# Kernel tuning notes

Measured on AMD Instinct MI355X. Metric: run time of the kernel, lower is better.

The kernel has to match this reference:

```python
import jax, jax.numpy as jnp
import numpy as np

DIM = 512
HEADS = 4
DH = 128          # dim_head
CHUNK = 16        # chunk_size
MAX_LR = 0.01     # default_adaptive_step_transform max_lr
EPS = 1e-6        # flax RMSNorm epsilon


def setup_inputs() -> dict:
    key = jax.random.key(0)
    ks = jax.random.split(key, 8)
    B, S = 2, 2048
    dim_inner = HEADS * DH
    seq = jax.random.normal(ks[0], (B, S, DIM), jnp.float32)
    store_norm_scale = jnp.ones((DIM,), jnp.float32)               # RMSNorm scale
    W_kv = (jax.random.normal(ks[1], (DIM, 2 * dim_inner)) * 0.02).astype(jnp.float32)
    W_step = (jax.random.normal(ks[2], (DIM, HEADS)) * 0.02).astype(jnp.float32)
    W_mom = (jax.random.normal(ks[3], (DIM, HEADS)) * 0.02).astype(jnp.float32)
    W_decay = (jax.random.normal(ks[4], (DIM, HEADS)) * 0.02).astype(jnp.float32)
    # past memory-MLP weights, shared init expanded to (b, h, dh, dh)
    w0 = jnp.broadcast_to((jax.random.normal(ks[5], (DH, DH)) * 0.02).astype(jnp.float32), (B, HEADS, DH, DH)) + 0.0
    w1 = jnp.broadcast_to((jax.random.normal(ks[6], (DH, DH)) * 0.02).astype(jnp.float32), (B, HEADS, DH, DH)) + 0.0
    return {"seq": seq, "store_norm_scale": store_norm_scale, "W_kv": W_kv,
            "W_step": W_step, "W_mom": W_mom, "W_decay": W_decay, "w0": w0, "w1": w1}


def _mlp(w0, w1, x):
    # MemoryMLP depth=2: x @ w0 ; silu ; @ w1
    return jax.nn.silu(x @ w0) @ w1


def _chunk_loss(w0, w1, k, lr, v):
    pred = _mlp(w0, w1, k)                       # [c, d]
    return jnp.sum(jnp.mean((pred - v) ** 2, axis=-1) * lr)


def _binop(e1, e2):
    a1, b1 = e1
    a2, b2 = e2
    return a1 * a2, a2 * b1 + b2


def _lin_scan(a, b):
    # first-order linear recurrence y_t = a_t * y_{t-1} + b_t along chunk axis (axis=2)
    return jax.lax.associative_scan(_binop, (a, b), axis=2)[1]


def _store(seq, store_norm_scale, W_kv, W_step, W_mom, W_decay, w0, w1):
    B, S, _ = seq.shape
    n = S // CHUNK
    # pre RMSNorm (with scale)
    x = seq * jax.lax.rsqrt(jnp.mean(seq * seq, axis=-1, keepdims=True) + EPS) * store_norm_scale
    # adaptive per-token lr:  sigmoid(x @ W_step) * max_lr  -> [b, h, s]
    lr = jax.nn.sigmoid(jnp.einsum('bsd,dh->bhs', x, W_step)) * MAX_LR
    # per-chunk mean -> momentum / decay factors  [b, h, n, 1]
    mean = x.reshape(B, n, CHUNK, DIM).mean(axis=2)
    mom = jax.nn.sigmoid(jnp.einsum('bnd,dh->bhn', mean, W_mom))[..., None]
    dec = jax.nn.sigmoid(jnp.einsum('bnd,dh->bhn', mean, W_decay))[..., None]
    # keys / values  [b*h, n, c, dh]
    kv = x @ W_kv
    k, v = jnp.split(kv, 2, axis=-1)
    k = k.reshape(B, n, CHUNK, HEADS, DH).transpose(0, 3, 1, 2, 4).reshape(B * HEADS, n, CHUNK, DH)
    v = v.reshape(B, n, CHUNK, HEADS, DH).transpose(0, 3, 1, 2, 4).reshape(B * HEADS, n, CHUNK, DH)
    lr_ch = lr.reshape(B, HEADS, n, CHUNK).reshape(B * HEADS, n, CHUNK)
    w0bh = w0.reshape(B * HEADS, DH, DH)
    w1bh = w1.reshape(B * HEADS, DH, DH)
    # per-chunk gradients of the MLP loss at the *past* weights (all chunks independent)
    gfn = jax.grad(_chunk_loss, argnums=(0, 1))
    gfn = jax.vmap(gfn, in_axes=(None, None, 0, 0, 0))   # over chunks n
    gfn = jax.vmap(gfn, in_axes=(0, 0, 0, 0, 0))         # over b*h
    g0, g1 = gfn(w0bh, w1bh, k, lr_ch, v)                # [b*h, n, dh, dh]
    s0 = (-g0).reshape(B, HEADS, n, DH * DH)             # surprises
    s1 = (-g1).reshape(B, HEADS, n, DH * DH)
    # momentum scan then decay scan (Titans update rule)
    m0 = _lin_scan(jnp.broadcast_to(mom, s0.shape), s0)
    m1 = _lin_scan(jnp.broadcast_to(mom, s1.shape), s1)
    u0 = _lin_scan(jnp.broadcast_to(1.0 - dec, m0.shape), m0)
    u1 = _lin_scan(jnp.broadcast_to(1.0 - dec, m1.shape), m1)
    updates = jnp.stack([u0.reshape(B, HEADS, n, DH, DH),
                         u1.reshape(B, HEADS, n, DH, DH)], axis=0)  # [2, b, h, n, dh, dh]
    return updates


def reference(seq, store_norm_scale, W_kv, W_step, W_mom, W_decay, w0, w1):
    return _store(seq, store_norm_scale, W_kv, W_step, W_mom, W_decay, w0, w1)
```

## Files before the change

### kernel.cpp

```cpp
#include <hip/hip_runtime.h>

#define DIMX 512
#define HEADSX 4
#define DHX 128
#define CHX 16
#define NCX 128
#define SX 2048
#define BX 2
#define BHX 8
#define PADX 520
#define PADF 136

typedef unsigned short ushort_t;
typedef unsigned int uint_t;
typedef short bf16x8 __attribute__((ext_vector_type(8)));
typedef float f32x4 __attribute__((ext_vector_type(4)));

__device__ __forceinline__ float sigmoidf_(float z){ return 1.0f/(1.0f + __expf(-z)); }

__device__ __forceinline__ ushort_t f2bf(float f){
  uint_t u = __float_as_uint(f);
  return (ushort_t)((u + 0x7FFFu + ((u >> 16) & 1u)) >> 16);
}
__device__ __forceinline__ uint_t pk2(float a, float b){
  return (uint_t)f2bf(a) | ((uint_t)f2bf(b) << 16);
}

__global__ __launch_bounds__(256) void k_prep(const float* __restrict__ Wkv,
    const float* __restrict__ w0, const float* __restrict__ w1,
    ushort_t* __restrict__ WkvT, ushort_t* __restrict__ w0T,
    ushort_t* __restrict__ w1T, ushort_t* __restrict__ w1n){
  int blk = blockIdx.x; int tid = threadIdx.x;
  if (blk < 64){
    int h = blk >> 4, kt = blk & 15;
    __shared__ ushort_t tile[256][33];
    for (int i=tid; i<8192; i+=256){
      int kk = i >> 8, col = i & 255;
      int wcol = (col < 128) ? (h*128 + col) : (384 + h*128 + col);
      float v = Wkv[(size_t)(kt*32+kk)*1024 + wcol];
      tile[col][kk] = f2bf(v);
    }
    __syncthreads();
    for (int i=tid; i<8192; i+=256){
      int col = i >> 5, kk = i & 31;
      WkvT[(((size_t)h*16 + kt)*256 + col)*32 + kk] = tile[col][kk];
    }
  } else {
    int bh = blk - 64;
    size_t base = (size_t)bh*16384;
    for (int i=tid; i<16384; i+=256){
      int r = i >> 7, c = i & 127;
      w0T[base + i] = f2bf(w0[base + (size_t)c*128 + r]);
      w1T[base + i] = f2bf(w1[base + (size_t)c*128 + r]);
      w1n[base + i] = f2bf(w1[base + i]);
    }
  }
}

__global__ __launch_bounds__(256) void k_fused2(const float* __restrict__ seq,
    const float* __restrict__ scale, const float* __restrict__ Wstep,
    const float* __restrict__ Wmom, const float* __restrict__ Wdec,
    const ushort_t* __restrict__ WkvT, const ushort_t* __restrict__ w0T,
    const ushort_t* __restrict__ w1T, const ushort_t* __restrict__ w1n,
    ushort_t* __restrict__ fac0, ushort_t* __restrict__ fac1,
    float* __restrict__ momw, float* __restrict__ decw){
  int blk = blockIdx.x;
  int bh = blk & 7, t = blk >> 3;
  int b = bh >> 2, h = bh & 3;
  int bt = bh*NCX + t;
  __shared__ __align__(16) ushort_t xs[16*PADX];
  __shared__ __align__(16) ushort_t ks[16*PADF];
  __shared__ __align__(16) ushort_t as_[16*PADF];
  __shared__ __align__(16) ushort_t dp_[16*PADF];
  __shared__ __align__(16) ushort_t dh_[16*PADF];
  __shared__ float red[4][8][4];
  __shared__ float rs_s[16], lr_s[16];
  int tid = threadIdx.x;
  int wv = tid>>6, lane = tid&63;
  int quad = lane>>4, nl = lane&15;
  const f32x4 zero = {0.f,0.f,0.f,0.f};

  const float4* sb = (const float4*)(seq + ((size_t)(b*SX + t*CHX))*DIMX);
  float4 q[8];
  #pragma unroll
  for (int it=0; it<8; it++) q[it] = sb[tid + 256*it];
  int k4 = tid & 127; int d0 = k4*4;
  float4 sc4 = *(const float4*)(scale + d0);
  float wsv[4], wmv[4], wdv[4];
  #pragma unroll
  for (int j=0;j<4;j++){
    wsv[j] = Wstep[(d0+j)*4 + h];
    wmv[j] = Wmom [(d0+j)*4 + h];
    wdv[j] = Wdec [(d0+j)*4 + h];
  }
  #pragma unroll
  for (int it=0; it<8; it++){
    float ssp = q[it].x*q[it].x + q[it].y*q[it].y + q[it].z*q[it].z + q[it].w*q[it].w;
    float xwx = q[it].x*sc4.x, xwy = q[it].y*sc4.y;
    float xwz = q[it].z*sc4.z, xww = q[it].w*sc4.w;
    float lp = xwx*wsv[0] + xwy*wsv[1] + xwz*wsv[2] + xww*wsv[3];
    float pm = xwx*wmv[0] + xwy*wmv[1] + xwz*wmv[2] + xww*wmv[3];
    float pd = xwx*wdv[0] + xwy*wdv[1] + xwz*wdv[2] + xww*wdv[3];
    #pragma unroll
    for (int o=32;o>0;o>>=1){
      ssp += __shfl_down(ssp,o,64); lp += __shfl_down(lp,o,64);
      pm  += __shfl_down(pm,o,64);  pd += __shfl_down(pd,o,64);
    }
    if (lane==0){ red[wv][it][0]=ssp; red[wv][it][1]=lp; red[wv][it][2]=pm; red[wv][it][3]=pd; }
  }
  __syncthreads();
  if (tid < 16){
    int c = tid;
    int w0i = (c & 1) ? 2 : 0;
    int iti = c >> 1;
    float ssc = red[w0i][iti][0] + red[w0i+1][iti][0];
    float lpc = red[w0i][iti][1] + red[w0i+1][iti][1];
    float pmc = red[w0i][iti][2] + red[w0i+1][iti][2];
    float pdc = red[w0i][iti][3] + red[w0i+1][iti][3];
    float rs = 1.0f / sqrtf(ssc*(1.0f/DIMX) + 1e-6f);
    rs_s[c] = rs;
    lr_s[c] = 0.01f * sigmoidf_(rs*lpc);
    float pmr = rs*pmc, pdr = rs*pdc;
    #pragma unroll
    for (int o=8;o>0;o>>=1){ pmr += __shfl_down(pmr,o,16); pdr += __shfl_down(pdr,o,16); }
    if (c==0){
      momw[bt] = sigmoidf_(pmr*(1.0f/CHX));
      decw[bt] = 1.0f - sigmoidf_(pdr*(1.0f/CHX));
    }
  }
  __syncthreads();
  #pragma unroll
  for (int it=0; it<8; it++){
    int f = tid + 256*it;
    int c = f >> 7;
    float rs = rs_s[c];
    uint2 u;
    u.x = pk2(q[it].x*rs*sc4.x, q[it].y*rs*sc4.y);
    u.y = pk2(q[it].z*rs*sc4.z, q[it].w*rs*sc4.w);
    *(uint2*)&xs[c*PADX + k4*4] = u;
  }
  __syncthreads();

  f32x4 kacc[2] = {zero, zero};
  f32x4 vacc[2] = {zero, zero};
  const ushort_t* wkvh = WkvT + (size_t)h*16*256*32;
  for (int kt=0; kt<16; kt++){
    bf16x8 Af = *(const bf16x8*)&xs[nl*PADX + kt*32 + quad*8];
    #pragma unroll
    for (int s=0; s<2; s++){
      int ktile = 2*wv + s;
      bf16x8 Bk = *(const bf16x8*)&wkvh[((size_t)kt*256 + (ktile*16+nl))*32 + quad*8];
      kacc[s] = __builtin_amdgcn_mfma_f32_16x16x32_bf16(Af, Bk, kacc[s], 0,0,0);
      int vtile = 8 + 2*wv + s;
      bf16x8 Bv = *(const bf16x8*)&wkvh[((size_t)kt*256 + (vtile*16+nl))*32 + quad*8];
      vacc[s] = __builtin_amdgcn_mfma_f32_16x16x32_bf16(Af, Bv, vacc[s], 0,0,0);
    }
  }
  #pragma unroll
  for (int s=0;s<2;s++){
    #pragma unroll
    for (int r=0;r<4;r++)
      ks[(quad*4+r)*PADF + 32*wv + 16*s + nl] = f2bf(kacc[s][r]);
  }
  __syncthreads();

  const ushort_t* w0b = w0T + (size_t)bh*16384;
  f32x4 hacc[2] = {zero, zero};
  for (int kt=0; kt<4; kt++){
    bf16x8 Af = *(const bf16x8*)&ks[nl*PADF + kt*32 + quad*8];
    #pragma unroll
    for (int s=0; s<2; s++){
      int n0 = (2*wv+s)*16;
      bf16x8 Bf = *(const bf16x8*)&w0b[(size_t)(n0+nl)*128 + kt*32 + quad*8];
      hacc[s] = __builtin_amdgcn_mfma_f32_16x16x32_bf16(Af, Bf, hacc[s], 0,0,0);
    }
  }
  float sp[2][4];
  #pragma unroll
  for (int s=0;s<2;s++){
    #pragma unroll
    for (int r=0;r<4;r++){
      float hh = hacc[s][r];
      float sg = sigmoidf_(hh);
      float a  = hh*sg;
      sp[s][r] = sg*(1.0f + hh*(1.0f-sg));
      as_[(quad*4+r)*PADF + 32*wv + 16*s + nl] = f2bf(a);
    }
  }
  __syncthreads();

  const ushort_t* w1tb = w1T + (size_t)bh*16384;
  f32x4 pacc[2] = {zero, zero};
  for (int kt=0; kt<4; kt++){
    bf16x8 Af = *(const bf16x8*)&as_[nl*PADF + kt*32 + quad*8];
    #pragma unroll
    for (int s=0; s<2; s++){
      int n0 = (2*wv+s)*16;
      bf16x8 Bf = *(const bf16x8*)&w1tb[(size_t)(n0+nl)*128 + kt*32 + quad*8];
      pacc[s] = __builtin_amdgcn_mfma_f32_16x16x32_bf16(Af, Bf, pacc[s], 0,0,0);
    }
  }
  float lrv[4];
  #pragma unroll
  for (int r=0;r<4;r++) lrv[r] = lr_s[quad*4 + r];
  #pragma unroll
  for (int s=0;s<2;s++){
    #pragma unroll
    for (int r=0;r<4;r++){
      float dp = (2.0f/DHX)*lrv[r]*(pacc[s][r] - vacc[s][r]);
      dp_[(quad*4+r)*PADF + 32*wv + 16*s + nl] = f2bf(dp);
    }
  }
  __syncthreads();

  const ushort_t* w1nb = w1n + (size_t)bh*16384;
  f32x4 dacc[2] = {zero, zero};
  for (int kt=0; kt<4; kt++){
    bf16x8 Af = *(const bf16x8*)&dp_[nl*PADF + kt*32 + quad*8];
    #pragma unroll
    for (int s=0; s<2; s++){
      int n0 = (2*wv+s)*16;
      bf16x8 Bf = *(const bf16x8*)&w1nb[(size_t)(n0+nl)*128 + kt*32 + quad*8];
      dacc[s] = __builtin_amdgcn_mfma_f32_16x16x32_bf16(Af, Bf, dacc[s], 0,0,0);
    }
  }
  #pragma unroll
  for (int s=0;s<2;s++){
    #pragma unroll
    for (int r=0;r<4;r++)
      dh_[(quad*4+r)*PADF + 32*wv + 16*s + nl] = f2bf(dacc[s][r]*sp[s][r]);
  }
  __syncthreads();

  {
    int p = tid & 127, which = tid >> 7;
    const ushort_t* s0 = which ? dh_ : ks;
    const ushort_t* s1 = which ? dp_ : as_;
    ushort_t rowv[32];
    #pragma unroll
    for (int c=0;c<16;c++){ rowv[c] = s0[c*PADF + p]; rowv[16+c] = s1[c*PADF + p]; }
    ushort_t* dst = (which ? fac1 : fac0) + ((size_t)bt*128 + p)*32;
    const uint4* rv = (const uint4*)rowv;
    uint4* dq = (uint4*)dst;
    dq[0]=rv[0]; dq[1]=rv[1]; dq[2]=rv[2]; dq[3]=rv[3];
  }
}

__global__ __launch_bounds__(64) void k_scan3(const ushort_t* __restrict__ fac0,
    const ushort_t* __restrict__ fac1,
    const float* __restrict__ momw, const float* __restrict__ decw,
    float* __restrict__ out){
  int blk = blockIdx.x;
  int bh  = blk & 7;
  int jb  = (blk >> 3) & 7;
  int ig  = (blk >> 6) & 7;
  int mat = blk >> 9;
  int lane = threadIdx.x;
  int quad = lane >> 4, rrow = lane & 15;
  const f32x4 zero = {0.f,0.f,0.f,0.f};
  const bf16x8 fz = {0,0,0,0,0,0,0,0};

  size_t rowbase = (size_t)bh*NCX*128;
  const ushort_t* pa = fac0 + (rowbase + (size_t)(ig*16 + rrow))*32 + mat*16 + quad*8;
  const ushort_t* pb = fac1 + (rowbase + (size_t)(jb*16 + rrow))*32 + mat*16 + quad*8;
  bool act = (quad < 2);

  bf16x8 fa0=fz, fb0=fz, fa1=fz, fb1=fz;
  if (act){
    fa0 = *(const bf16x8*)(pa);
    fb0 = *(const bf16x8*)(pb);
    fa1 = *(const bf16x8*)(pa + 4096);
    fb1 = *(const bf16x8*)(pb + 4096);
  }

  f32x4 m_ = zero, u_ = zero;
  size_t obase = ((size_t)(mat*BHX + bh)*NCX)*((size_t)DHX*DHX)
               + (size_t)(ig*16 + quad*4)*DHX + (size_t)(jb*16 + rrow);
  const float* mop = momw + bh*NCX;
  const float* dep = decw + bh*NCX;

  for (int t=0; t<NCX; t+=2){
    bf16x8 na0=fz, nb0=fz, na1=fz, nb1=fz;
    if (act && (t+2 < NCX)){
      na0 = *(const bf16x8*)(pa + (size_t)(t+2)*4096);
      nb0 = *(const bf16x8*)(pb + (size_t)(t+2)*4096);
      na1 = *(const bf16x8*)(pa + (size_t)(t+3)*4096);
      nb1 = *(const bf16x8*)(pb + (size_t)(t+3)*4096);
    }
    float mo = mop[t], de = dep[t];
    f32x4 g = __builtin_amdgcn_mfma_f32_16x16x32_bf16(fa0, fb0, zero, 0,0,0);
    float* ob = out + obase + (size_t)t*(DHX*DHX);
    #pragma unroll
    for (int r=0;r<4;r++){
      m_[r] = mo*m_[r] - g[r];
      u_[r] = de*u_[r] + m_[r];
      ob[(size_t)r*DHX] = u_[r];
    }
    mo = mop[t+1]; de = dep[t+1];
    g = __builtin_amdgcn_mfma_f32_16x16x32_bf16(fa1, fb1, zero, 0,0,0);
    ob += (size_t)DHX*DHX;
    #pragma unroll
    for (int r=0;r<4;r++){
      m_[r] = mo*m_[r] - g[r];
      u_[r] = de*u_[r] + m_[r];
      ob[(size_t)r*DHX] = u_[r];
    }
    fa0=na0; fb0=nb0; fa1=na1; fb1=nb1;
  }
}

extern "C" void kernel_launch(void* const* d_in, const int* in_sizes, int n_in,
                              void* d_out, int out_size, void* d_ws, size_t ws_size,
                              hipStream_t stream) {
  (void)in_sizes; (void)n_in; (void)out_size; (void)ws_size;
  const float* seq   = (const float*)d_in[0];
  const float* scale = (const float*)d_in[1];
  const float* Wkv   = (const float*)d_in[2];
  const float* Wstep = (const float*)d_in[3];
  const float* Wmom  = (const float*)d_in[4];
  const float* Wdec  = (const float*)d_in[5];
  const float* w0    = (const float*)d_in[6];
  const float* w1    = (const float*)d_in[7];
  float* out = (float*)d_out;

  ushort_t* fac0 = (ushort_t*)d_ws;
  ushort_t* fac1 = fac0 + 4194304;
  ushort_t* WkvT = fac1 + 4194304;
  ushort_t* w0T  = WkvT + 524288;
  ushort_t* w1T  = w0T + 131072;
  ushort_t* w1n  = w1T + 131072;
  float*    momw = (float*)(w1n + 131072);
  float*    decw = momw + 1024;

  k_prep<<<dim3(72), dim3(256), 0, stream>>>(Wkv, w0, w1, WkvT, w0T, w1T, w1n);
  k_fused2<<<dim3(BHX*NCX), dim3(256), 0, stream>>>(seq, scale, Wstep, Wmom, Wdec,
      WkvT, w0T, w1T, w1n, fac0, fac1, momw, decw);
  k_scan3<<<dim3(1024), dim3(64), 0, stream>>>(fac0, fac1, momw, decw, out);
}
```

Measured before the change: 233.7 us.

## Assign one chunk per wavefront and drop block-level syncs in fused gradient kernel

The fused per-chunk gradient kernel changes from one 256-thread block per chunk, with four waves splitting the N dimension and synchronizing between stages, to one chunk per wavefront with four chunks per block. Each wave now computes all 128 output columns on its own and uses a private LDS slice, so every __syncthreads is removed. RMSNorm statistics are computed from register loads instead of an LDS staging buffer. The norm scale is folded into the pre-transposed weights in the prep kernel. The cost is far more accumulator registers per wave (8 tiles for each of k, v, h, p and d), which can lower occupancy. The grid also shrinks to 256 blocks, and the weight B-fragments are re-read from global memory by every wave.

Result: slower. 244.0 us (+4.4%).

```diff
diff --git a/kernel.cpp b/kernel.cpp
--- a/kernel.cpp
+++ b/kernel.cpp
@@ -8,7 +8,6 @@
 #define SX 2048
 #define BX 2
 #define BHX 8
-#define PADX 520
 #define PADF 136
 
 typedef unsigned short ushort_t;
@@ -28,16 +27,21 @@
 
 __global__ __launch_bounds__(256) void k_prep(const float* __restrict__ Wkv,
     const float* __restrict__ w0, const float* __restrict__ w1,
+    const float* __restrict__ scale,
+    const float* __restrict__ Wstep, const float* __restrict__ Wmom,
+    const float* __restrict__ Wdec,
     ushort_t* __restrict__ WkvT, ushort_t* __restrict__ w0T,
-    ushort_t* __restrict__ w1T, ushort_t* __restrict__ w1n){
+    ushort_t* __restrict__ w1T, ushort_t* __restrict__ w1n,
+    float* __restrict__ wfsS, float* __restrict__ wfsM, float* __restrict__ wfsD){
   int blk = blockIdx.x; int tid = threadIdx.x;
   if (blk < 64){
     int h = blk >> 4, kt = blk & 15;
     __shared__ ushort_t tile[256][33];
     for (int i=tid; i<8192; i+=256){
       int kk = i >> 8, col = i & 255;
+      int d = kt*32 + kk;
       int wcol = (col < 128) ? (h*128 + col) : (384 + h*128 + col);
-      float v = Wkv[(size_t)(kt*32+kk)*1024 + wcol];
+      float v = scale[d] * Wkv[(size_t)d*1024 + wcol];
       tile[col][kk] = f2bf(v);
     }
     __syncthreads();
@@ -45,7 +49,7 @@
       int col = i >> 5, kk = i & 31;
       WkvT[(((size_t)h*16 + kt)*256 + col)*32 + kk] = tile[col][kk];
     }
-  } else {
+  } else if (blk < 72){
     int bh = blk - 64;
     size_t base = (size_t)bh*16384;
     for (int i=tid; i<16384; i+=256){
@@ -54,195 +58,202 @@
       w1T[base + i] = f2bf(w1[base + (size_t)c*128 + r]);
       w1n[base + i] = f2bf(w1[base + i]);
     }
-  }
-}
-
-__global__ __launch_bounds__(256) void k_fused2(const float* __restrict__ seq,
-    const float* __restrict__ scale, const float* __restrict__ Wstep,
-    const float* __restrict__ Wmom, const float* __restrict__ Wdec,
+  } else {
+    for (int i=tid; i<2048; i+=256){
+      int d = i & 511, h = i >> 9;
+      float sc = scale[d];
+      wfsS[i] = sc * Wstep[d*4 + h];
+      wfsM[i] = sc * Wmom [d*4 + h];
+      wfsD[i] = sc * Wdec [d*4 + h];
+    }
+  }
+}
+
+__global__ __launch_bounds__(256) void k_fused3(const float* __restrict__ seq,
+    const float* __restrict__ wfsS, const float* __restrict__ wfsM,
+    const float* __restrict__ wfsD,
     const ushort_t* __restrict__ WkvT, const ushort_t* __restrict__ w0T,
     const ushort_t* __restrict__ w1T, const ushort_t* __restrict__ w1n,
     ushort_t* __restrict__ fac0, ushort_t* __restrict__ fac1,
     float* __restrict__ momw, float* __restrict__ decw){
   int blk = blockIdx.x;
-  int bh = blk & 7, t = blk >> 3;
+  int bh = blk & 7, tq = blk >> 3;
   int b = bh >> 2, h = bh & 3;
+  int tid = threadIdx.x;
+  int wv = tid >> 6, lane = tid & 63;
+  int t = tq*4 + wv;
   int bt = bh*NCX + t;
-  __shared__ __align__(16) ushort_t xs[16*PADX];
-  __shared__ __align__(16) ushort_t ks[16*PADF];
-  __shared__ __align__(16) ushort_t as_[16*PADF];
-  __shared__ __align__(16) ushort_t dp_[16*PADF];
-  __shared__ __align__(16) ushort_t dh_[16*PADF];
-  __shared__ float red[4][8][4];
-  __shared__ float rs_s[16], lr_s[16];
-  int tid = threadIdx.x;
-  int wv = tid>>6, lane = tid&63;
-  int quad = lane>>4, nl = lane&15;
+  int quad = lane >> 4, nl = lane & 15;
   const f32x4 zero = {0.f,0.f,0.f,0.f};
 
-  const float4* sb = (const float4*)(seq + ((size_t)(b*SX + t*CHX))*DIMX);
-  float4 q[8];
-  #pragma unroll
-  for (int it=0; it<8; it++) q[it] = sb[tid + 256*it];
-  int k4 = tid & 127; int d0 = k4*4;
-  float4 sc4 = *(const float4*)(scale + d0);
-  float wsv[4], wmv[4], wdv[4];
-  #pragma unroll
-  for (int j=0;j<4;j++){
-    wsv[j] = Wstep[(d0+j)*4 + h];
-    wmv[j] = Wmom [(d0+j)*4 + h];
-    wdv[j] = Wdec [(d0+j)*4 + h];
-  }
-  #pragma unroll
-  for (int it=0; it<8; it++){
-    float ssp = q[it].x*q[it].x + q[it].y*q[it].y + q[it].z*q[it].z + q[it].w*q[it].w;
-    float xwx = q[it].x*sc4.x, xwy = q[it].y*sc4.y;
-    float xwz = q[it].z*sc4.z, xww = q[it].w*sc4.w;
-    float lp = xwx*wsv[0] + xwy*wsv[1] + xwz*wsv[2] + xww*wsv[3];
-    float pm = xwx*wmv[0] + xwy*wmv[1] + xwz*wmv[2] + xww*wmv[3];
-    float pd = xwx*wdv[0] + xwy*wdv[1] + xwz*wdv[2] + xww*wdv[3];
-    #pragma unroll
-    for (int o=32;o>0;o>>=1){
-      ssp += __shfl_down(ssp,o,64); lp += __shfl_down(lp,o,64);
-      pm  += __shfl_down(pm,o,64);  pd += __shfl_down(pd,o,64);
-    }
-    if (lane==0){ red[wv][it][0]=ssp; red[wv][it][1]=lp; red[wv][it][2]=pm; red[wv][it][3]=pd; }
-  }
-  __syncthreads();
-  if (tid < 16){
-    int c = tid;
-    int w0i = (c & 1) ? 2 : 0;
-    int iti = c >> 1;
-    float ssc = red[w0i][iti][0] + red[w0i+1][iti][0];
-    float lpc = red[w0i][iti][1] + red[w0i+1][iti][1];
-    float pmc = red[w0i][iti][2] + red[w0i+1][iti][2];
-    float pdc = red[w0i][iti][3] + red[w0i+1][iti][3];
-    float rs = 1.0f / sqrtf(ssc*(1.0f/DIMX) + 1e-6f);
-    rs_s[c] = rs;
-    lr_s[c] = 0.01f * sigmoidf_(rs*lpc);
-    float pmr = rs*pmc, pdr = rs*pdc;
-    #pragma unroll
-    for (int o=8;o>0;o>>=1){ pmr += __shfl_down(pmr,o,16); pdr += __shfl_down(pdr,o,16); }
-    if (c==0){
-      momw[bt] = sigmoidf_(pmr*(1.0f/CHX));
-      decw[bt] = 1.0f - sigmoidf_(pdr*(1.0f/CHX));
-    }
-  }
-  __syncthreads();
-  #pragma unroll
-  for (int it=0; it<8; it++){
-    int f = tid + 256*it;
-    int c = f >> 7;
-    float rs = rs_s[c];
-    uint2 u;
-    u.x = pk2(q[it].x*rs*sc4.x, q[it].y*rs*sc4.y);
-    u.y = pk2(q[it].z*rs*sc4.z, q[it].w*rs*sc4.w);
-    *(uint2*)&xs[c*PADX + k4*4] = u;
-  }
-  __syncthreads();
-
-  f32x4 kacc[2] = {zero, zero};
-  f32x4 vacc[2] = {zero, zero};
+  __shared__ __align__(16) ushort_t ks_[4][16*PADF];
+  __shared__ __align__(16) ushort_t as_[4][16*PADF];
+  __shared__ __align__(16) ushort_t dp_[4][16*PADF];
+  __shared__ __align__(16) ushort_t dh_[4][16*PADF];
+  __shared__ float lr_s[4][16];
+  ushort_t* ksw = ks_[wv]; ushort_t* asw = as_[wv];
+  ushort_t* dpw = dp_[wv]; ushort_t* dhw = dh_[wv];
+
+  const float* sq = seq + ((size_t)(b*SX + t*CHX) + nl)*DIMX + quad*8;
+  const float* wS = wfsS + h*512 + quad*8;
+  const float* wM = wfsM + h*512 + quad*8;
+  const float* wD = wfsD + h*512 + quad*8;
+
+  float ss=0.f, lp=0.f, pm=0.f, pd=0.f;
+  #pragma unroll
+  for (int kt=0; kt<16; kt++){
+    float4 q0 = *(const float4*)(sq + kt*32);
+    float4 q1 = *(const float4*)(sq + kt*32 + 4);
+    float4 s0 = *(const float4*)(wS + kt*32);
+    float4 s1 = *(const float4*)(wS + kt*32 + 4);
+    float4 m0 = *(const float4*)(wM + kt*32);
+    float4 m1 = *(const float4*)(wM + kt*32 + 4);
+    float4 d0 = *(const float4*)(wD + kt*32);
+    float4 d1 = *(const float4*)(wD + kt*32 + 4);
+    ss += q0.x*q0.x + q0.y*q0.y + q0.z*q0.z + q0.w*q0.w
+        + q1.x*q1.x + q1.y*q1.y + q1.z*q1.z + q1.w*q1.w;
+    lp += q0.x*s0.x + q0.y*s0.y + q0.z*s0.z + q0.w*s0.w
+        + q1.x*s1.x + q1.y*s1.y + q1.z*s1.z + q1.w*s1.w;
+    pm += q0.x*m0.x + q0.y*m0.y + q0.z*m0.z + q0.w*m0.w
+        + q1.x*m1.x + q1.y*m1.y + q1.z*m1.z + q1.w*m1.w;
+    pd += q0.x*d0.x + q0.y*d0.y + q0.z*d0.z + q0.w*d0.w
+        + q1.x*d1.x + q1.y*d1.y + q1.z*d1.z + q1.w*d1.w;
+  }
+  #pragma unroll
+  for (int mk=16; mk<64; mk<<=1){
+    ss += __shfl_xor(ss, mk, 64); lp += __shfl_xor(lp, mk, 64);
+    pm += __shfl_xor(pm, mk, 64); pd += __shfl_xor(pd, mk, 64);
+  }
+  float rs = 1.0f / sqrtf(ss*(1.0f/DIMX) + 1e-6f);
+  float lr = 0.01f * sigmoidf_(rs*lp);
+  float pmr = rs*pm, pdr = rs*pd;
+  #pragma unroll
+  for (int mk=1; mk<16; mk<<=1){
+    pmr += __shfl_xor(pmr, mk, 64); pdr += __shfl_xor(pdr, mk, 64);
+  }
+  if (lane==0){
+    momw[bt] = sigmoidf_(pmr*(1.0f/CHX));
+    decw[bt] = 1.0f - sigmoidf_(pdr*(1.0f/CHX));
+  }
+  if (quad==0) lr_s[wv][nl] = lr;
+
+  union BF { bf16x8 v; uint_t u[4]; };
+  f32x4 kacc[8], vacc[8];
+  #pragma unroll
+  for (int s=0;s<8;s++){ kacc[s]=zero; vacc[s]=zero; }
   const ushort_t* wkvh = WkvT + (size_t)h*16*256*32;
   for (int kt=0; kt<16; kt++){
-    bf16x8 Af = *(const bf16x8*)&xs[nl*PADX + kt*32 + quad*8];
-    #pragma unroll
-    for (int s=0; s<2; s++){
-      int ktile = 2*wv + s;
-      bf16x8 Bk = *(const bf16x8*)&wkvh[((size_t)kt*256 + (ktile*16+nl))*32 + quad*8];
-      kacc[s] = __builtin_amdgcn_mfma_f32_16x16x32_bf16(Af, Bk, kacc[s], 0,0,0);
-      int vtile = 8 + 2*wv + s;
-      bf16x8 Bv = *(const bf16x8*)&wkvh[((size_t)kt*256 + (vtile*16+nl))*32 + quad*8];
-      vacc[s] = __builtin_amdgcn_mfma_f32_16x16x32_bf16(Af, Bv, vacc[s], 0,0,0);
-    }
-  }
-  #pragma unroll
-  for (int s=0;s<2;s++){
+    float4 q0 = *(const float4*)(sq + kt*32);
+    float4 q1 = *(const float4*)(sq + kt*32 + 4);
+    BF af;
+    af.u[0] = pk2(q0.x*rs, q0.y*rs);
+    af.u[1] = pk2(q0.z*rs, q0.w*rs);
+    af.u[2] = pk2(q1.x*rs, q1.y*rs);
+    af.u[3] = pk2(q1.z*rs, q1.w*rs);
+    const ushort_t* wb = wkvh + ((size_t)kt*256 + nl)*32 + quad*8;
+    #pragma unroll
+    for (int s=0; s<8; s++){
+      bf16x8 Bk = *(const bf16x8*)(wb + (size_t)(s*16)*32);
+      kacc[s] = __builtin_amdgcn_mfma_f32_16x16x32_bf16(af.v, Bk, kacc[s], 0,0,0);
+      bf16x8 Bv = *(const bf16x8*)(wb + (size_t)(128 + s*16)*32);
+      vacc[s] = __builtin_amdgcn_mfma_f32_16x16x32_bf16(af.v, Bv, vacc[s], 0,0,0);
+    }
+  }
+  #pragma unroll
+  for (int s=0;s<8;s++){
     #pragma unroll
     for (int r=0;r<4;r++)
-      ks[(quad*4+r)*PADF + 32*wv + 16*s + nl] = f2bf(kacc[s][r]);
-  }
-  __syncthreads();
+      ksw[(quad*4+r)*PADF + s*16 + nl] = f2bf(kacc[s][r]);
+  }
 
   const ushort_t* w0b = w0T + (size_t)bh*16384;
-  f32x4 hacc[2] = {zero, zero};
+  f32x4 hacc[8];
+  #pragma unroll
+  for (int s=0;s<8;s++) hacc[s]=zero;
   for (int kt=0; kt<4; kt++){
-    bf16x8 Af = *(const bf16x8*)&ks[nl*PADF + kt*32 + quad*8];
-    #pragma unroll
-    for (int s=0; s<2; s++){
-      int n0 = (2*wv+s)*16;
-      bf16x8 Bf = *(const bf16x8*)&w0b[(size_t)(n0+nl)*128 + kt*32 + quad*8];
+    bf16x8 Af = *(const bf16x8*)&ksw[nl*PADF + kt*32 + quad*8];
+    #pragma unroll
+    for (int s=0; s<8; s++){
+      bf16x8 Bf = *(const bf16x8*)&w0b[(size_t)(s*16+nl)*128 + kt*32 + quad*8];
       hacc[s] = __builtin_amdgcn_mfma_f32_16x16x32_bf16(Af, Bf, hacc[s], 0,0,0);
     }
   }
-  float sp[2][4];
-  #pragma unroll
-  for (int s=0;s<2;s++){
+  float sp[8][4];
+  #pragma unroll
+  for (int s=0;s<8;s++){
     #pragma unroll
     for (int r=0;r<4;r++){
       float hh = hacc[s][r];
       float sg = sigmoidf_(hh);
       float a  = hh*sg;
       sp[s][r] = sg*(1.0f + hh*(1.0f-sg));
-      as_[(quad*4+r)*PADF + 32*wv + 16*s + nl] = f2bf(a);
-    }
-  }
-  __syncthreads();
+      asw[(quad*4+r)*PADF + s*16 + nl] = f2bf(a);
+    }
+  }
 
   const ushort_t* w1tb = w1T + (size_t)bh*16384;
-  f32x4 pacc[2] = {zero, zero};
+  f32x4 pacc[8];
+  #pragma unroll
+  for (int s=0;s<8;s++) pacc[s]=zero;
   for (int kt=0; kt<4; kt++){
-    bf16x8 Af = *(const bf16x8*)&as_[nl*PADF + kt*32 + quad*8];
-    #pragma unroll
-    for (int s=0; s<2; s++){
-      int n0 = (2*wv+s)*16;
-      bf16x8 Bf = *(const bf16x8*)&w1tb[(size_t)(n0+nl)*128 + kt*32 + quad*8];
+    bf16x8 Af = *(const bf16x8*)&asw[nl*PADF + kt*32 + quad*8];
+    #pragma unroll
+    for (int s=0; s<8; s++){
+      bf16x8 Bf = *(const bf16x8*)&w1tb[(size_t)(s*16+nl)*128 + kt*32 + quad*8];
       pacc[s] = __builtin_amdgcn_mfma_f32_16x16x32_bf16(Af, Bf, pacc[s], 0,0,0);
     }
   }
   float lrv[4];
   #pragma unroll
-  for (int r=0;r<4;r++) lrv[r] = lr_s[quad*4 + r];
-  #pragma unroll
-  for (int s=0;s<2;s++){
+  for (int r=0;r<4;r++) lrv[r] = lr_s[wv][quad*4 + r];
+  #pragma unroll
+  for (int s=0;s<8;s++){
     #pragma unroll
     for (int r=0;r<4;r++){
       float dp = (2.0f/DHX)*lrv[r]*(pacc[s][r] - vacc[s][r]);
-      dp_[(quad*4+r)*PADF + 32*wv + 16*s + nl] = f2bf(dp);
-    }
-  }
-  __syncthreads();
+      dpw[(quad*4+r)*PADF + s*16 + nl] = f2bf(dp);
+    }
+  }
 
   const ushort_t* w1nb = w1n + (size_t)bh*16384;
-  f32x4 dacc[2] = {zero, zero};
+  f32x4 dacc[8];
+  #pragma unroll
+  for (int s=0;s<8;s++) dacc[s]=zero;
   for (int kt=0; kt<4; kt++){
-    bf16x8 Af = *(const bf16x8*)&dp_[nl*PADF + kt*32 + quad*8];
-    #pragma unroll
-    for (int s=0; s<2; s++){
-      int n0 = (2*wv+s)*16;
-      bf16x8 Bf = *(const bf16x8*)&w1nb[(size_t)(n0+nl)*128 + kt*32 + quad*8];
+    bf16x8 Af = *(const bf16x8*)&dpw[nl*PADF + kt*32 + quad*8];
+    #pragma unroll
+    for (int s=0; s<8; s++){
+      bf16x8 Bf = *(const bf16x8*)&w1nb[(size_t)(s*16+nl)*128 + kt*32 + quad*8];
       dacc[s] = __builtin_amdgcn_mfma_f32_16x16x32_bf16(Af, Bf, dacc[s], 0,0,0);
     }
   }
   #pragma unroll
-  for (int s=0;s<2;s++){
+  for (int s=0;s<8;s++){
     #pragma unroll
     for (int r=0;r<4;r++)
-      dh_[(quad*4+r)*PADF + 32*wv + 16*s + nl] = f2bf(dacc[s][r]*sp[s][r]);
-  }
-  __syncthreads();
-
-  {
-    int p = tid & 127, which = tid >> 7;
-    const ushort_t* s0 = which ? dh_ : ks;
-    const ushort_t* s1 = which ? dp_ : as_;
+      dhw[(quad*4+r)*PADF + s*16 + nl] = f2bf(dacc[s][r]*sp[s][r]);
+  }
+
+  #pragma unroll
+  for (int j=0;j<2;j++){
+    int p = lane + j*64;
     ushort_t rowv[32];
     #pragma unroll
-    for (int c=0;c<16;c++){ rowv[c] = s0[c*PADF + p]; rowv[16+c] = s1[c*PADF + p]; }
-    ushort_t* dst = (which ? fac1 : fac0) + ((size_t)bt*128 + p)*32;
-    const uint4* rv = (const uint4*)rowv;
-    uint4* dq = (uint4*)dst;
-    dq[0]=rv[0]; dq[1]=rv[1]; dq[2]=rv[2]; dq[3]=rv[3];
+    for (int c=0;c<16;c++){ rowv[c] = ksw[c*PADF + p]; rowv[16+c] = asw[c*PADF + p]; }
+    {
+      ushort_t* dst = fac0 + ((size_t)bt*128 + p)*32;
+      const uint4* rv = (const uint4*)rowv;
+      uint4* dq = (uint4*)dst;
+      dq[0]=rv[0]; dq[1]=rv[1]; dq[2]=rv[2]; dq[3]=rv[3];
+    }
+    #pragma unroll
+    for (int c=0;c<16;c++){ rowv[c] = dhw[c*PADF + p]; rowv[16+c] = dpw[c*PADF + p]; }
+    {
+      ushort_t* dst = fac1 + ((size_t)bt*128 + p)*32;
+      const uint4* rv = (const uint4*)rowv;
+      uint4* dq = (uint4*)dst;
+      dq[0]=rv[0]; dq[1]=rv[1]; dq[2]=rv[2]; dq[3]=rv[3];
+    }
   }
 }
 
@@ -331,9 +342,13 @@
   ushort_t* w1n  = w1T + 131072;
   float*    momw = (float*)(w1n + 131072);
   float*    decw = momw + 1024;
-
-  k_prep<<<dim3(72), dim3(256), 0, stream>>>(Wkv, w0, w1, WkvT, w0T, w1T, w1n);
-  k_fused2<<<dim3(BHX*NCX), dim3(256), 0, stream>>>(seq, scale, Wstep, Wmom, Wdec,
+  float*    wfsS = decw + 1024;
+  float*    wfsM = wfsS + 2048;
+  float*    wfsD = wfsM + 2048;
+
+  k_prep<<<dim3(73), dim3(256), 0, stream>>>(Wkv, w0, w1, scale, Wstep, Wmom, Wdec,
+      WkvT, w0T, w1T, w1n, wfsS, wfsM, wfsD);
+  k_fused3<<<dim3(256), dim3(256), 0, stream>>>(seq, wfsS, wfsM, wfsD,
       WkvT, w0T, w1T, w1n, fac0, fac1, momw, decw);
   k_scan3<<<dim3(1024), dim3(64), 0, stream>>>(fac0, fac1, momw, decw, out);
 }
```

## Process four chunks per 1024-thread block and prefold norm scale into gate weights

Applied to the files above, without the earlier changes.

The fused gradient kernel now runs 1024 threads per block, handling four chunks of the same batch-head in one block, with each group of four waves owning one chunk. The norm scale is multiplied into the step, momentum and decay weights once in the prep kernel, so the per-token reductions no longer apply it. The dh_ shared buffer is dropped by reusing ks, and the fac0 write-out is moved earlier. The intent is to share weight-tile cache traffic across chunks and cut barrier and launch overhead. In exchange the block needs much more LDS and occupancy per CU drops, and every __syncthreads now spans 16 waves.

Result: no change. 236.0 us (+1.0%).

```diff
diff --git a/kernel.cpp b/kernel.cpp
--- a/kernel.cpp
+++ b/kernel.cpp
@@ -28,8 +28,12 @@
 
 __global__ __launch_bounds__(256) void k_prep(const float* __restrict__ Wkv,
     const float* __restrict__ w0, const float* __restrict__ w1,
+    const float* __restrict__ scale,
+    const float* __restrict__ Wstep, const float* __restrict__ Wmom,
+    const float* __restrict__ Wdec,
     ushort_t* __restrict__ WkvT, ushort_t* __restrict__ w0T,
-    ushort_t* __restrict__ w1T, ushort_t* __restrict__ w1n){
+    ushort_t* __restrict__ w1T, ushort_t* __restrict__ w1n,
+    float* __restrict__ wfsS, float* __restrict__ wfsM, float* __restrict__ wfsD){
   int blk = blockIdx.x; int tid = threadIdx.x;
   if (blk < 64){
     int h = blk >> 4, kt = blk & 15;
@@ -45,7 +49,7 @@
       int col = i >> 5, kk = i & 31;
       WkvT[(((size_t)h*16 + kt)*256 + col)*32 + kk] = tile[col][kk];
     }
-  } else {
+  } else if (blk < 72){
     int bh = blk - 64;
     size_t base = (size_t)bh*16384;
     for (int i=tid; i<16384; i+=256){
@@ -54,104 +58,102 @@
       w1T[base + i] = f2bf(w1[base + (size_t)c*128 + r]);
       w1n[base + i] = f2bf(w1[base + i]);
     }
-  }
-}
-
-__global__ __launch_bounds__(256) void k_fused2(const float* __restrict__ seq,
-    const float* __restrict__ scale, const float* __restrict__ Wstep,
-    const float* __restrict__ Wmom, const float* __restrict__ Wdec,
+  } else {
+    for (int i=tid; i<2048; i+=256){
+      int d = i & 511, h = i >> 9;
+      float sc = scale[d];
+      wfsS[i] = sc * Wstep[d*4 + h];
+      wfsM[i] = sc * Wmom [d*4 + h];
+      wfsD[i] = sc * Wdec [d*4 + h];
+    }
+  }
+}
+
+__global__ __launch_bounds__(1024, 4) void k_fused5(const float* __restrict__ seq,
+    const float* __restrict__ scale,
+    const float* __restrict__ wfsS, const float* __restrict__ wfsM,
+    const float* __restrict__ wfsD,
     const ushort_t* __restrict__ WkvT, const ushort_t* __restrict__ w0T,
     const ushort_t* __restrict__ w1T, const ushort_t* __restrict__ w1n,
     ushort_t* __restrict__ fac0, ushort_t* __restrict__ fac1,
     float* __restrict__ momw, float* __restrict__ decw){
   int blk = blockIdx.x;
-  int bh = blk & 7, t = blk >> 3;
+  int bh = blk & 7, t4 = blk >> 3;
   int b = bh >> 2, h = bh & 3;
+  int tid = threadIdx.x;
+  int wv = tid >> 6;
+  int mi = wv >> 2, ni = wv & 3;
+  int lane = tid & 63;
+  int quad = lane >> 4, nl = lane & 15;
+  int tid_g = ni*64 + lane;
+  int t = t4*4 + mi;
   int bt = bh*NCX + t;
-  __shared__ __align__(16) ushort_t xs[16*PADX];
-  __shared__ __align__(16) ushort_t ks[16*PADF];
-  __shared__ __align__(16) ushort_t as_[16*PADF];
-  __shared__ __align__(16) ushort_t dp_[16*PADF];
-  __shared__ __align__(16) ushort_t dh_[16*PADF];
-  __shared__ float red[4][8][4];
-  __shared__ float rs_s[16], lr_s[16];
-  int tid = threadIdx.x;
-  int wv = tid>>6, lane = tid&63;
-  int quad = lane>>4, nl = lane&15;
   const f32x4 zero = {0.f,0.f,0.f,0.f};
 
-  const float4* sb = (const float4*)(seq + ((size_t)(b*SX + t*CHX))*DIMX);
-  float4 q[8];
-  #pragma unroll
-  for (int it=0; it<8; it++) q[it] = sb[tid + 256*it];
-  int k4 = tid & 127; int d0 = k4*4;
-  float4 sc4 = *(const float4*)(scale + d0);
-  float wsv[4], wmv[4], wdv[4];
-  #pragma unroll
-  for (int j=0;j<4;j++){
-    wsv[j] = Wstep[(d0+j)*4 + h];
-    wmv[j] = Wmom [(d0+j)*4 + h];
-    wdv[j] = Wdec [(d0+j)*4 + h];
-  }
-  #pragma unroll
-  for (int it=0; it<8; it++){
-    float ssp = q[it].x*q[it].x + q[it].y*q[it].y + q[it].z*q[it].z + q[it].w*q[it].w;
-    float xwx = q[it].x*sc4.x, xwy = q[it].y*sc4.y;
-    float xwz = q[it].z*sc4.z, xww = q[it].w*sc4.w;
-    float lp = xwx*wsv[0] + xwy*wsv[1] + xwz*wsv[2] + xww*wsv[3];
-    float pm = xwx*wmv[0] + xwy*wmv[1] + xwz*wmv[2] + xww*wmv[3];
-    float pd = xwx*wdv[0] + xwy*wdv[1] + xwz*wdv[2] + xww*wdv[3];
-    #pragma unroll
-    for (int o=32;o>0;o>>=1){
-      ssp += __shfl_down(ssp,o,64); lp += __shfl_down(lp,o,64);
-      pm  += __shfl_down(pm,o,64);  pd += __shfl_down(pd,o,64);
-    }
-    if (lane==0){ red[wv][it][0]=ssp; red[wv][it][1]=lp; red[wv][it][2]=pm; red[wv][it][3]=pd; }
-  }
-  __syncthreads();
-  if (tid < 16){
-    int c = tid;
-    int w0i = (c & 1) ? 2 : 0;
-    int iti = c >> 1;
-    float ssc = red[w0i][iti][0] + red[w0i+1][iti][0];
-    float lpc = red[w0i][iti][1] + red[w0i+1][iti][1];
-    float pmc = red[w0i][iti][2] + red[w0i+1][iti][2];
-    float pdc = red[w0i][iti][3] + red[w0i+1][iti][3];
-    float rs = 1.0f / sqrtf(ssc*(1.0f/DIMX) + 1e-6f);
-    rs_s[c] = rs;
-    lr_s[c] = 0.01f * sigmoidf_(rs*lpc);
-    float pmr = rs*pmc, pdr = rs*pdc;
-    #pragma unroll
-    for (int o=8;o>0;o>>=1){ pmr += __shfl_down(pmr,o,16); pdr += __shfl_down(pdr,o,16); }
-    if (c==0){
-      momw[bt] = sigmoidf_(pmr*(1.0f/CHX));
-      decw[bt] = 1.0f - sigmoidf_(pdr*(1.0f/CHX));
-    }
-  }
-  __syncthreads();
-  #pragma unroll
-  for (int it=0; it<8; it++){
-    int f = tid + 256*it;
-    int c = f >> 7;
-    float rs = rs_s[c];
-    uint2 u;
-    u.x = pk2(q[it].x*rs*sc4.x, q[it].y*rs*sc4.y);
-    u.y = pk2(q[it].z*rs*sc4.z, q[it].w*rs*sc4.w);
-    *(uint2*)&xs[c*PADX + k4*4] = u;
-  }
-  __syncthreads();
-
-  f32x4 kacc[2] = {zero, zero};
-  f32x4 vacc[2] = {zero, zero};
+  __shared__ __align__(16) ushort_t xs[4][16*PADX];
+  __shared__ __align__(16) ushort_t ks[4][16*PADF];
+  __shared__ __align__(16) ushort_t as_[4][16*PADF];
+  __shared__ __align__(16) ushort_t dp_[4][16*PADF];
+  __shared__ float lr_s[4][16];
+  __shared__ float red_m[4][4], red_d[4][4];
+
+  {
+    int c = tid_g >> 4, sl = tid_g & 15;
+    const float4* sr = (const float4*)(seq + ((size_t)(b*SX + t*CHX) + c)*DIMX);
+    const float4* scl = (const float4*)scale;
+    const float4* wS = (const float4*)(wfsS + h*512);
+    const float4* wM = (const float4*)(wfsM + h*512);
+    const float4* wD = (const float4*)(wfsD + h*512);
+    float4 q[8];
+    #pragma unroll
+    for (int jj=0; jj<8; jj++) q[jj] = sr[sl + 16*jj];
+    float ss=0.f, lp=0.f, pm=0.f, pd=0.f;
+    #pragma unroll
+    for (int jj=0; jj<8; jj++){
+      float4 a = q[jj];
+      float4 s4 = wS[sl+16*jj], m4 = wM[sl+16*jj], d4 = wD[sl+16*jj];
+      ss += a.x*a.x + a.y*a.y + a.z*a.z + a.w*a.w;
+      lp += a.x*s4.x + a.y*s4.y + a.z*s4.z + a.w*s4.w;
+      pm += a.x*m4.x + a.y*m4.y + a.z*m4.z + a.w*m4.w;
+      pd += a.x*d4.x + a.y*d4.y + a.z*d4.z + a.w*d4.w;
+    }
+    #pragma unroll
+    for (int mk=1; mk<16; mk<<=1){
+      ss += __shfl_xor(ss,mk,64); lp += __shfl_xor(lp,mk,64);
+      pm += __shfl_xor(pm,mk,64); pd += __shfl_xor(pd,mk,64);
+    }
+    float rs = 1.0f / sqrtf(ss*(1.0f/DIMX) + 1e-6f);
+    if (sl==0) lr_s[mi][c] = 0.01f * sigmoidf_(rs*lp);
+    float pmr = rs*pm, pdr = rs*pd;
+    #pragma unroll
+    for (int mk=16; mk<64; mk<<=1){ pmr += __shfl_xor(pmr,mk,64); pdr += __shfl_xor(pdr,mk,64); }
+    if (lane==0){ red_m[mi][ni]=pmr; red_d[mi][ni]=pdr; }
+    #pragma unroll
+    for (int jj=0; jj<8; jj++){
+      float4 s4 = scl[sl+16*jj];
+      uint2 u;
+      u.x = pk2(q[jj].x*rs*s4.x, q[jj].y*rs*s4.y);
+      u.y = pk2(q[jj].z*rs*s4.z, q[jj].w*rs*s4.w);
+      *(uint2*)&xs[mi][c*PADX + (sl+16*jj)*4] = u;
+    }
+  }
+  __syncthreads();
+  if (tid_g==0){
+    momw[bt] = sigmoidf_((red_m[mi][0]+red_m[mi][1]+red_m[mi][2]+red_m[mi][3])*(1.0f/CHX));
+    decw[bt] = 1.0f - sigmoidf_((red_d[mi][0]+red_d[mi][1]+red_d[mi][2]+red_d[mi][3])*(1.0f/CHX));
+  }
+
+  f32x4 kacc[2] = {zero,zero};
+  f32x4 vacc[2] = {zero,zero};
   const ushort_t* wkvh = WkvT + (size_t)h*16*256*32;
   for (int kt=0; kt<16; kt++){
-    bf16x8 Af = *(const bf16x8*)&xs[nl*PADX + kt*32 + quad*8];
+    bf16x8 Af = *(const bf16x8*)&xs[mi][nl*PADX + kt*32 + quad*8];
     #pragma unroll
     for (int s=0; s<2; s++){
-      int ktile = 2*wv + s;
+      int ktile = 2*ni + s;
       bf16x8 Bk = *(const bf16x8*)&wkvh[((size_t)kt*256 + (ktile*16+nl))*32 + quad*8];
       kacc[s] = __builtin_amdgcn_mfma_f32_16x16x32_bf16(Af, Bk, kacc[s], 0,0,0);
-      int vtile = 8 + 2*wv + s;
+      int vtile = 8 + 2*ni + s;
       bf16x8 Bv = *(const bf16x8*)&wkvh[((size_t)kt*256 + (vtile*16+nl))*32 + quad*8];
       vacc[s] = __builtin_amdgcn_mfma_f32_16x16x32_bf16(Af, Bv, vacc[s], 0,0,0);
     }
@@ -160,17 +162,18 @@
   for (int s=0;s<2;s++){
     #pragma unroll
     for (int r=0;r<4;r++)
-      ks[(quad*4+r)*PADF + 32*wv + 16*s + nl] = f2bf(kacc[s][r]);
+      ks[mi][(quad*4+r)*PADF + 32*ni + 16*s + nl] = f2bf(kacc[s][r]);
   }
   __syncthreads();
 
   const ushort_t* w0b = w0T + (size_t)bh*16384;
-  f32x4 hacc[2] = {zero, zero};
+  f32x4 hacc[2] = {zero,zero};
+  #pragma unroll
   for (int kt=0; kt<4; kt++){
-    bf16x8 Af = *(const bf16x8*)&ks[nl*PADF + kt*32 + quad*8];
+    bf16x8 Af = *(const bf16x8*)&ks[mi][nl*PADF + kt*32 + quad*8];
     #pragma unroll
     for (int s=0; s<2; s++){
-      int n0 = (2*wv+s)*16;
+      int n0 = (2*ni+s)*16;
       bf16x8 Bf = *(const bf16x8*)&w0b[(size_t)(n0+nl)*128 + kt*32 + quad*8];
       hacc[s] = __builtin_amdgcn_mfma_f32_16x16x32_bf16(Af, Bf, hacc[s], 0,0,0);
     }
@@ -182,44 +185,54 @@
     for (int r=0;r<4;r++){
       float hh = hacc[s][r];
       float sg = sigmoidf_(hh);
-      float a  = hh*sg;
       sp[s][r] = sg*(1.0f + hh*(1.0f-sg));
-      as_[(quad*4+r)*PADF + 32*wv + 16*s + nl] = f2bf(a);
+      as_[mi][(quad*4+r)*PADF + 32*ni + 16*s + nl] = f2bf(hh*sg);
     }
   }
   __syncthreads();
 
   const ushort_t* w1tb = w1T + (size_t)bh*16384;
-  f32x4 pacc[2] = {zero, zero};
+  f32x4 pacc[2] = {zero,zero};
+  #pragma unroll
   for (int kt=0; kt<4; kt++){
-    bf16x8 Af = *(const bf16x8*)&as_[nl*PADF + kt*32 + quad*8];
+    bf16x8 Af = *(const bf16x8*)&as_[mi][nl*PADF + kt*32 + quad*8];
     #pragma unroll
     for (int s=0; s<2; s++){
-      int n0 = (2*wv+s)*16;
+      int n0 = (2*ni+s)*16;
       bf16x8 Bf = *(const bf16x8*)&w1tb[(size_t)(n0+nl)*128 + kt*32 + quad*8];
       pacc[s] = __builtin_amdgcn_mfma_f32_16x16x32_bf16(Af, Bf, pacc[s], 0,0,0);
     }
   }
   float lrv[4];
   #pragma unroll
-  for (int r=0;r<4;r++) lrv[r] = lr_s[quad*4 + r];
+  for (int r=0;r<4;r++) lrv[r] = lr_s[mi][quad*4 + r];
   #pragma unroll
   for (int s=0;s<2;s++){
     #pragma unroll
     for (int r=0;r<4;r++){
       float dp = (2.0f/DHX)*lrv[r]*(pacc[s][r] - vacc[s][r]);
-      dp_[(quad*4+r)*PADF + 32*wv + 16*s + nl] = f2bf(dp);
-    }
+      dp_[mi][(quad*4+r)*PADF + 32*ni + 16*s + nl] = f2bf(dp);
+    }
+  }
+  if (tid_g < 128){
+    int p = tid_g;
+    ushort_t rowv[32];
+    #pragma unroll
+    for (int c=0;c<16;c++){ rowv[c] = ks[mi][c*PADF + p]; rowv[16+c] = as_[mi][c*PADF + p]; }
+    uint4* dq = (uint4*)(fac0 + ((size_t)bt*128 + p)*32);
+    const uint4* rv = (const uint4*)rowv;
+    dq[0]=rv[0]; dq[1]=rv[1]; dq[2]=rv[2]; dq[3]=rv[3];
   }
   __syncthreads();
 
   const ushort_t* w1nb = w1n + (size_t)bh*16384;
-  f32x4 dacc[2] = {zero, zero};
+  f32x4 dacc[2] = {zero,zero};
+  #pragma unroll
   for (int kt=0; kt<4; kt++){
-    bf16x8 Af = *(const bf16x8*)&dp_[nl*PADF + kt*32 + quad*8];
+    bf16x8 Af = *(const bf16x8*)&dp_[mi][nl*PADF + kt*32 + quad*8];
     #pragma unroll
     for (int s=0; s<2; s++){
-      int n0 = (2*wv+s)*16;
+      int n0 = (2*ni+s)*16;
       bf16x8 Bf = *(const bf16x8*)&w1nb[(size_t)(n0+nl)*128 + kt*32 + quad*8];
       dacc[s] = __builtin_amdgcn_mfma_f32_16x16x32_bf16(Af, Bf, dacc[s], 0,0,0);
     }
@@ -228,20 +241,17 @@
   for (int s=0;s<2;s++){
     #pragma unroll
     for (int r=0;r<4;r++)
-      dh_[(quad*4+r)*PADF + 32*wv + 16*s + nl] = f2bf(dacc[s][r]*sp[s][r]);
-  }
-  __syncthreads();
-
-  {
-    int p = tid & 127, which = tid >> 7;
-    const ushort_t* s0 = which ? dh_ : ks;
-    const ushort_t* s1 = which ? dp_ : as_;
+      ks[mi][(quad*4+r)*PADF + 32*ni + 16*s + nl] = f2bf(dacc[s][r]*sp[s][r]);
+  }
+  __syncthreads();
+
+  if (tid_g < 128){
+    int p = tid_g;
     ushort_t rowv[32];
     #pragma unroll
-    for (int c=0;c<16;c++){ rowv[c] = s0[c*PADF + p]; rowv[16+c] = s1[c*PADF + p]; }
-    ushort_t* dst = (which ? fac1 : fac0) + ((size_t)bt*128 + p)*32;
+    for (int c=0;c<16;c++){ rowv[c] = ks[mi][c*PADF + p]; rowv[16+c] = dp_[mi][c*PADF + p]; }
+    uint4* dq = (uint4*)(fac1 + ((size_t)bt*128 + p)*32);
     const uint4* rv = (const uint4*)rowv;
-    uint4* dq = (uint4*)dst;
     dq[0]=rv[0]; dq[1]=rv[1]; dq[2]=rv[2]; dq[3]=rv[3];
   }
 }
@@ -322,18 +332,23 @@
   const float* w0    = (const float*)d_in[6];
   const float* w1    = (const float*)d_in[7];
   float* out = (float*)d_out;
-
-  ushort_t* fac0 = (ushort_t*)d_ws;
-  ushort_t* fac1 = fac0 + 4194304;
-  ushort_t* WkvT = fac1 + 4194304;
-  ushort_t* w0T  = WkvT + 524288;
-  ushort_t* w1T  = w0T + 131072;
-  ushort_t* w1n  = w1T + 131072;
-  float*    momw = (float*)(w1n + 131072);
-  float*    decw = momw + 1024;
-
-  k_prep<<<dim3(72), dim3(256), 0, stream>>>(Wkv, w0, w1, WkvT, w0T, w1T, w1n);
-  k_fused2<<<dim3(BHX*NCX), dim3(256), 0, stream>>>(seq, scale, Wstep, Wmom, Wdec,
+  float* ws  = (float*)d_ws;
+
+  ushort_t* fac0 = (ushort_t*)(ws);
+  ushort_t* fac1 = (ushort_t*)(ws + 2097152);
+  ushort_t* WkvT = (ushort_t*)(ws + 4194304);
+  ushort_t* w0T  = (ushort_t*)(ws + 4456448);
+  ushort_t* w1T  = (ushort_t*)(ws + 4521984);
+  ushort_t* w1n  = (ushort_t*)(ws + 4587520);
+  float*    momw = ws + 4653056;
+  float*    decw = ws + 4654080;
+  float*    wfsS = ws + 4655104;
+  float*    wfsM = ws + 4657152;
+  float*    wfsD = ws + 4659200;
+
+  k_prep<<<dim3(73), dim3(256), 0, stream>>>(Wkv, w0, w1, scale, Wstep, Wmom, Wdec,
+      WkvT, w0T, w1T, w1n, wfsS, wfsM, wfsD);
+  k_fused5<<<dim3(256), dim3(1024), 0, stream>>>(seq, scale, wfsS, wfsM, wfsD,
       WkvT, w0T, w1T, w1n, fac0, fac1, momw, decw);
   k_scan3<<<dim3(1024), dim3(64), 0, stream>>>(fac0, fac1, momw, decw, out);
 }
```
